# Kernel tuning notes

Measured on AMD Instinct MI355X. Metric: run time of the kernel, lower is better.

The kernel has to match this reference:

```python
import jax, jax.numpy as jnp
import numpy as np

B, S, D, K, F = 4, 2048, 1024, 4, 4096
C_COEF = 8.0  # RG-LRU gating exponent from Griffin paper
EPS = 1e-6


def setup_inputs() -> dict:
    key = jax.random.key(0)
    ks = jax.random.split(key, 12)
    def n(k, shape, scale=1.0):
        return jax.random.normal(k, shape, dtype=jnp.float32) * scale
    sd = 1.0 / np.sqrt(D)
    return {
        "x": n(ks[0], (B, S, D)),
        "velocity": n(ks[1], (B, S, D), 0.1),
        "pre_norm_w": jnp.ones((D,), jnp.float32),
        "conv_kernel": n(ks[2], (D, K), 0.3),   # depthwise causal conv weights
        "conv_bias": jnp.zeros((D,), jnp.float32),
        "W_gate": n(ks[3], (D, D), sd),
        "W_a": n(ks[4], (D, D), sd),
        "lam": n(ks[5], (D,)),
        "W_out": n(ks[6], (2 * D, D), 1.0 / np.sqrt(2 * D)),
        "b_out": jnp.zeros((D,), jnp.float32),
        "log_beta": n(ks[7], (D,), 0.5),
        "ffn_norm_w": jnp.ones((D,), jnp.float32),
        "W_ff1": n(ks[8], (D, F), sd),
        "b_ff1": jnp.zeros((F,), jnp.float32),
        "W_ff2": n(ks[9], (F, D), 1.0 / np.sqrt(F)),
        "b_ff2": jnp.zeros((D,), jnp.float32),
    }


def _rmsnorm(x, w):
    # matches: rsqrt(x.float().pow(2).mean(-1, keepdim=True) + 1e-6); cast back; * weight
    xf = x.astype(jnp.float32)
    rms = jax.lax.rsqrt(jnp.mean(xf * xf, axis=-1, keepdims=True) + EPS)
    return (xf * rms).astype(x.dtype) * w


def _causal_dwconv(x, kernel, bias):
    # y[b,t,d] = bias[d] + sum_k kernel[d,k] * x[b,t-k,d]  (causal depthwise)
    k_taps = kernel.shape[1]
    s = x.shape[1]
    pad = jnp.pad(x, ((0, 0), (k_taps - 1, 0), (0, 0)))
    out = bias
    for k in range(k_taps):  # tiny fixed loop over kernel taps
        out = out + pad[:, k_taps - 1 - k : k_taps - 1 - k + s, :] * kernel[:, k]
    return out


def _griffin_scan(x, W_gate, W_a, lam):
    # RG-LRU: h_t = a_t * h_{t-1} + sqrt(1 - a_t^2) * (i_t * x_t)
    gate = jax.nn.sigmoid(jnp.einsum("bsd,de->bse", x, W_gate))
    log_a = -C_COEF * jax.nn.softplus(lam) * jax.nn.sigmoid(
        jnp.einsum("bsd,de->bse", x, W_a)
    )  # [B,S,D], log_a <= 0
    a = jnp.exp(log_a)
    u = jnp.sqrt(jnp.maximum(1.0 - a * a, 0.0)) * (gate * x)

    def step(h, au):
        a_t, u_t = au
        h = a_t * h + u_t
        return h, h

    a_t = jnp.moveaxis(a, 1, 0)  # [S,B,D]
    u_t = jnp.moveaxis(u, 1, 0)
    h0 = jnp.zeros_like(a_t[0])
    _, hs = jax.lax.scan(step, h0, (a_t, u_t))
    return jnp.moveaxis(hs, 0, 1)  # [B,S,D]


def reference(x, velocity, pre_norm_w, conv_kernel, conv_bias, W_gate, W_a, lam,
              W_out, b_out, log_beta, ffn_norm_w, W_ff1, b_ff1, W_ff2, b_ff2):
    x_norm = _rmsnorm(x, pre_norm_w)
    conv_out = _causal_dwconv(x_norm, conv_kernel, conv_bias)
    griffin_out = _griffin_scan(x_norm, W_gate, W_a, lam)
    mixer_out = jnp.concatenate([conv_out, griffin_out], axis=-1) @ W_out + b_out
    beta = jax.nn.sigmoid(log_beta)
    velocity = beta * velocity + mixer_out
    x = x + velocity
    normed = _rmsnorm(x, ffn_norm_w)
    ffn = jax.nn.gelu(normed @ W_ff1 + b_ff1) @ W_ff2 + b_ff2
    return (x + ffn, velocity)
```

## Files before the change

kernel.cpp:

```cpp
#include <hip/hip_runtime.h>

static constexpr int Bb = 4;
static constexpr int Ss = 2048;
static constexpr int Dd = 1024;
static constexpr int Ff = 4096;
static constexpr int Mm = Bb * Ss;
static constexpr size_t ND = (size_t)Mm * Dd;
static constexpr int CH = 32;
static constexpr int CL = Ss / CH;

typedef __attribute__((ext_vector_type(8))) short short8;
typedef __attribute__((ext_vector_type(4))) float floatx4;

__device__ __forceinline__ unsigned f2bf(float f) {
  unsigned u = __builtin_bit_cast(unsigned, f);
  return (u + 0x7FFFu + ((u >> 16) & 1u)) >> 16;
}
__device__ __forceinline__ float bf2f(unsigned bits) {
  return __builtin_bit_cast(float, bits << 16);
}
__device__ __forceinline__ void gload_lds16(const void* g, void* lds) {
  __builtin_amdgcn_global_load_lds((const __attribute__((address_space(1))) void*)g,
                                   (__attribute__((address_space(3))) void*)lds,
                                   16, 0, 0);
}
__device__ __forceinline__ float fsig(float x) {
  return __builtin_amdgcn_rcpf(1.0f + __expf(-x));
}
__device__ __forceinline__ float fgelu(float v) {
  float z = 1.5957691216057308f * fmaf(0.044715f * v, v * v, v);
  return v * __builtin_amdgcn_rcpf(1.0f + __expf(-z));
}

__global__ __launch_bounds__(256) void wconv_k(const float* __restrict__ W,
                                               unsigned short* __restrict__ WT,
                                               int K, int N) {
  __shared__ float tile[32][33];
  int tx = threadIdx.x & 31, ty = threadIdx.x >> 5;
  int bx = blockIdx.x * 32, by = blockIdx.y * 32;
#pragma unroll
  for (int i = 0; i < 32; i += 8)
    tile[ty + i][tx] = W[(size_t)(by + ty + i) * N + bx + tx];
  __syncthreads();
#pragma unroll
  for (int i = 0; i < 32; i += 8)
    WT[(size_t)(bx + ty + i) * K + by + tx] = (unsigned short)f2bf(tile[tx][ty + i]);
}

__global__ __launch_bounds__(256) void rmsnorm_bf_k(const float* __restrict__ x,
                                                    const float* __restrict__ w,
                                                    unsigned short* __restrict__ out) {
  int row = blockIdx.x;
  const float4* xr = (const float4*)(x + (size_t)row * Dd);
  int t = threadIdx.x;
  float4 v = xr[t];
  float ss = v.x * v.x + v.y * v.y + v.z * v.z + v.w * v.w;
#pragma unroll
  for (int off = 32; off > 0; off >>= 1) ss += __shfl_down(ss, off, 64);
  __shared__ float sb[4];
  if ((t & 63) == 0) sb[t >> 6] = ss;
  __syncthreads();
  float tot = sb[0] + sb[1] + sb[2] + sb[3];
  float sc = rsqrtf(tot * (1.0f / (float)Dd) + 1e-6f);
  float4 wv = ((const float4*)w)[t];
  unsigned lo = f2bf(v.x * sc * wv.x) | (f2bf(v.y * sc * wv.y) << 16);
  unsigned hi = f2bf(v.z * sc * wv.z) | (f2bf(v.w * sc * wv.w) << 16);
  *(uint2*)(out + (size_t)row * Dd + t * 4) = make_uint2(lo, hi);
}

__global__ __launch_bounds__(256) void conv_k(const unsigned short* __restrict__ xn,
                                              const float* __restrict__ kern,
                                              const float* __restrict__ bias,
                                              unsigned short* __restrict__ outC) {
  size_t q = (size_t)blockIdx.x * 256 + threadIdx.x;
  size_t i = q * 4;
  int d = (int)(i & (Dd - 1));
  int m = (int)(i >> 10);
  int t = m & (Ss - 1);
  float acc[4];
#pragma unroll
  for (int j = 0; j < 4; j++) acc[j] = bias[d + j];
#pragma unroll
  for (int k = 0; k < 4; k++) {
    if (t >= k) {
      uint2 xv = *(const uint2*)(xn + i - (size_t)k * Dd);
      float x0 = bf2f(xv.x & 0xFFFF), x1 = bf2f(xv.x >> 16);
      float x2 = bf2f(xv.y & 0xFFFF), x3 = bf2f(xv.y >> 16);
      acc[0] = fmaf(kern[(d + 0) * 4 + k], x0, acc[0]);
      acc[1] = fmaf(kern[(d + 1) * 4 + k], x1, acc[1]);
      acc[2] = fmaf(kern[(d + 2) * 4 + k], x2, acc[2]);
      acc[3] = fmaf(kern[(d + 3) * 4 + k], x3, acc[3]);
    }
  }
  unsigned lo = f2bf(acc[0]) | (f2bf(acc[1]) << 16);
  unsigned hi = f2bf(acc[2]) | (f2bf(acc[3]) << 16);
  *(uint2*)(outC + (size_t)m * (2 * Dd) + d) = make_uint2(lo, hi);
}

template <int MODE>
__global__ __launch_bounds__(512, 2) void bgemm3_k(const unsigned short* __restrict__ A,
                                                   const unsigned short* __restrict__ BT,
                                                   void* __restrict__ Cout,
                                                   int M, int N, int K,
                                                   const float* __restrict__ bias,
                                                   const float* __restrict__ extra,
                                                   const float* __restrict__ vel_in,
                                                   const float* __restrict__ x_in,
                                                   const float* __restrict__ log_beta,
                                                   float* __restrict__ vel_out) {
  __shared__ unsigned short LA[2][256 * 64];
  __shared__ unsigned short LB[2][256 * 64];
  const int tid = threadIdx.x;
  const int wid = tid >> 6, lane = tid & 63;
  const int wm = wid >> 2, wn = wid & 3;
  const int r = lane & 15, quad = lane >> 4, r7 = lane & 7;

  const int gx = gridDim.x;
  int id = blockIdx.y * gx + blockIdx.x;
  const int nwg = gx * gridDim.y;
  id = (id & 7) * (nwg >> 3) + (id >> 3);
  const int bm = (id / gx) * 256, bn = (id % gx) * 256;
  const int NIT = K >> 7;

  const int lrow = lane >> 3;
  const int sblk = (lane & 7) ^ lrow;
  const unsigned short* AsrcB = A  + (size_t)(bm + lrow) * K + sblk * 8;
  const unsigned short* BsrcB = BT + (size_t)(bn + lrow) * K + sblk * 8;

  const int aB = wm * 8192 + r * 64;
  const int bB = wn * 4096 + r * 64;
  const int kq0 = (quad ^ r7) * 8;
  const int kq1 = ((4 + quad) ^ r7) * 8;

  floatx4 acc[8][4];
#pragma unroll
  for (int i = 0; i < 8; i++)
#pragma unroll
    for (int j = 0; j < 4; j++) acc[i][j] = (floatx4){0.f, 0.f, 0.f, 0.f};

#define STG_A(bq, k0, h, s)                                                           \
  gload_lds16(AsrcB + (size_t)((h) * 128 + (s) * 64 + wid * 8) * K + (k0),            \
              (void*)&LA[bq][((h) * 128 + (s) * 64 + wid * 8) * 64])
#define STG_B(bq, k0, h, s)                                                           \
  gload_lds16(BsrcB + (size_t)((h) * 128 + (s) * 64 + wid * 8) * K + (k0),            \
              (void*)&LB[bq][((h) * 128 + (s) * 64 + wid * 8) * 64])
#define RDA(il, IH, buf)                                                              \
  aF[il][0] = *(const short8*)&LA[buf][aB + (IH) * 4096 + (il) * 1024 + kq0];         \
  aF[il][1] = *(const short8*)&LA[buf][aB + (IH) * 4096 + (il) * 1024 + kq1]
#define RDB(BF, jl, jg, buf)                                                          \
  BF[jl][0] = *(const short8*)&LB[buf][bB + (jg) * 1024 + kq0];                       \
  BF[jl][1] = *(const short8*)&LB[buf][bB + (jg) * 1024 + kq1]
#define MM2(il, jl, BF, IH, JH)                                                       \
  acc[(IH) * 4 + (il)][(JH) * 2 + (jl)] = __builtin_amdgcn_mfma_f32_16x16x32_bf16(    \
      BF[jl][0], aF[il][0], acc[(IH) * 4 + (il)][(JH) * 2 + (jl)], 0, 0, 0);          \
  acc[(IH) * 4 + (il)][(JH) * 2 + (jl)] = __builtin_amdgcn_mfma_f32_16x16x32_bf16(    \
      BF[jl][1], aF[il][1], acc[(IH) * 4 + (il)][(JH) * 2 + (jl)], 0, 0, 0)
#define MQUAD(BF, IH, JH)                                                             \
  MM2(0, 0, BF, IH, JH); MM2(0, 1, BF, IH, JH); MM2(1, 0, BF, IH, JH);                \
  MM2(1, 1, BF, IH, JH); MM2(2, 0, BF, IH, JH); MM2(2, 1, BF, IH, JH);                \
  MM2(3, 0, BF, IH, JH); MM2(3, 1, BF, IH, JH)
#define BAR() __builtin_amdgcn_s_barrier()
#define LGK0()                                                                        \
  asm volatile("s_waitcnt lgkmcnt(0)" ::: "memory");                                  \
  __builtin_amdgcn_sched_barrier(0)
#define PRIO(x) __builtin_amdgcn_s_setprio(x)

  STG_A(0, 0, 0, 0); STG_A(0, 0, 0, 1); STG_A(0, 0, 1, 0); STG_A(0, 0, 1, 1);
  STG_B(0, 0, 0, 0); STG_B(0, 0, 0, 1); STG_B(0, 0, 1, 0); STG_B(0, 0, 1, 1);
  STG_B(1, 64, 0, 0); STG_B(1, 64, 0, 1); STG_B(1, 64, 1, 0); STG_B(1, 64, 1, 1);
  asm volatile("s_waitcnt vmcnt(4)" ::: "memory");
  BAR();
  __builtin_amdgcn_sched_barrier(0);

  for (int it = 0; it < NIT; ++it) {
    const int T = 2 * it;
    const int pf = (it + 1 < NIT);
    const int kA1 = (T + 1) << 6;
    const int k2 = (T + 2) << 6, k3 = (T + 3) << 6;
    short8 aF[4][2], b0[2][2], b1[2][2];

    STG_A(1, kA1, 0, 0); STG_A(1, kA1, 0, 1);
    RDA(0, 0, 0); RDA(1, 0, 0); RDA(2, 0, 0); RDA(3, 0, 0);
    RDB(b0, 0, 0, 0); RDB(b0, 1, 1, 0);
    BAR(); LGK0();
    PRIO(1); MQUAD(b0, 0, 0); PRIO(0);
    BAR();

    STG_A(1, kA1, 1, 0); STG_A(1, kA1, 1, 1);
    RDB(b1, 0, 2, 0); RDB(b1, 1, 3, 0);
    BAR(); LGK0();
    PRIO(1); MQUAD(b1, 0, 1); PRIO(0);
    BAR();

    if (pf) { STG_B(0, k2, 0, 0); STG_B(0, k2, 0, 1); }
    RDA(0, 1, 0); RDA(1, 1, 0); RDA(2, 1, 0); RDA(3, 1, 0);
    BAR(); LGK0();
    PRIO(1); MQUAD(b0, 1, 0); PRIO(0);
    BAR();

    if (pf) { STG_B(0, k2, 1, 0); STG_B(0, k2, 1, 1); }
    BAR();
    PRIO(1); MQUAD(b1, 1, 1); PRIO(0);
    if (pf) asm volatile("s_waitcnt vmcnt(4)" ::: "memory");
    else    asm volatile("s_waitcnt vmcnt(0)" ::: "memory");
    BAR();
    __builtin_amdgcn_sched_barrier(0);

    if (pf) { STG_A(0, k2, 0, 0); STG_A(0, k2, 0, 1); }
    RDA(0, 0, 1); RDA(1, 0, 1); RDA(2, 0, 1); RDA(3, 0, 1);
    RDB(b0, 0, 0, 1); RDB(b0, 1, 1, 1);
    BAR(); LGK0();
    PRIO(1); MQUAD(b0, 0, 0); PRIO(0);
    BAR();

    if (pf) { STG_A(0, k2, 1, 0); STG_A(0, k2, 1, 1); }
    RDB(b1, 0, 2, 1); RDB(b1, 1, 3, 1);
    BAR(); LGK0();
    PRIO(1); MQUAD(b1, 0, 1); PRIO(0);
    BAR();

    if (pf) { STG_B(1, k3, 0, 0); STG_B(1, k3, 0, 1); }
    RDA(0, 1, 1); RDA(1, 1, 1); RDA(2, 1, 1); RDA(3, 1, 1);
    BAR(); LGK0();
    PRIO(1); MQUAD(b0, 1, 0); PRIO(0);
    BAR();

    if (pf) { STG_B(1, k3, 1, 0); STG_B(1, k3, 1, 1); }
    BAR();
    PRIO(1); MQUAD(b1, 1, 1); PRIO(0);
    if (pf) {
      asm volatile("s_waitcnt vmcnt(4)" ::: "memory");
      BAR();
      __builtin_amdgcn_sched_barrier(0);
    }
  }
#undef STG_A
#undef STG_B
#undef RDA
#undef RDB
#undef MM2
#undef MQUAD
#undef BAR
#undef LGK0
#undef PRIO

#pragma unroll
  for (int i = 0; i < 8; i++) {
    int rowg = bm + wm * 128 + i * 16 + r;
#pragma unroll
    for (int j = 0; j < 4; j++) {
      int colg = bn + wn * 64 + j * 16 + quad * 4;
      size_t idx = (size_t)rowg * N + colg;
      float v0 = acc[i][j][0], v1 = acc[i][j][1], v2 = acc[i][j][2], v3 = acc[i][j][3];
      if (MODE & 1) {
        float4 bv = *(const float4*)(bias + colg);
        v0 += bv.x; v1 += bv.y; v2 += bv.z; v3 += bv.w;
      }
      if (MODE & 2) {
        v0 = fgelu(v0); v1 = fgelu(v1); v2 = fgelu(v2); v3 = fgelu(v3);
      }
      if (MODE & 4) {
        float4 ev = *(const float4*)(extra + idx);
        v0 += ev.x; v1 += ev.y; v2 += ev.z; v3 += ev.w;
      }
      if (MODE & 16) {
        float4 lb = *(const float4*)(log_beta + colg);
        float4 vi = *(const float4*)(vel_in + idx);
        float4 xi = *(const float4*)(x_in + idx);
        float4 vn;
        vn.x = fmaf(fsig(lb.x), vi.x, v0);
        vn.y = fmaf(fsig(lb.y), vi.y, v1);
        vn.z = fmaf(fsig(lb.z), vi.z, v2);
        vn.w = fmaf(fsig(lb.w), vi.w, v3);
        *(float4*)(vel_out + idx) = vn;
        v0 = xi.x + vn.x; v1 = xi.y + vn.y; v2 = xi.z + vn.z; v3 = xi.w + vn.w;
      }
      if (MODE & 8) {
        uint2 pk;
        pk.x = f2bf(v0) | (f2bf(v1) << 16);
        pk.y = f2bf(v2) | (f2bf(v3) << 16);
        *(uint2*)((unsigned short*)Cout + idx) = pk;
      } else {
        float4 o; o.x = v0; o.y = v1; o.z = v2; o.w = v3;
        *(float4*)((float*)Cout + idx) = o;
      }
    }
  }
}

__global__ __launch_bounds__(256) void scan_p1(const unsigned short* __restrict__ gapre,
                                               const unsigned short* __restrict__ xn,
                                               const float* __restrict__ lam,
                                               unsigned short* __restrict__ ub,
                                               float* __restrict__ carryA,
                                               float* __restrict__ carryH) {
  int g = blockIdx.x * 256 + threadIdx.x;
  int e = g & (Dd - 1);
  int bc = g >> 10;
  int b = bc & 3;
  int c = bc >> 2;
  float l = lam[e];
  float sp = fmaxf(l, 0.0f) + log1pf(__expf(-fabsf(l)));
  float m8sp = -8.0f * sp;
  size_t m0 = (size_t)b * Ss + (size_t)c * CL;
  float A = 1.0f, h = 0.0f;
#pragma unroll 4
  for (int t = 0; t < CL; t++) {
    size_t m = m0 + t;
    float gp = bf2f(gapre[m * 2048 + e]);
    float ap = bf2f(gapre[m * 2048 + 1024 + e]);
    float xv = bf2f(xn[m * Dd + e]);
    float a = __expf(m8sp * fsig(ap));
    float u = sqrtf(fmaxf(1.0f - a * a, 0.0f)) * fsig(gp) * xv;
    ub[m * Dd + e] = (unsigned short)f2bf(u);
    A *= a;
    h = fmaf(a, h, u);
  }
  carryA[c * 4096 + b * 1024 + e] = A;
  carryH[c * 4096 + b * 1024 + e] = h;
}

__global__ __launch_bounds__(256) void scan_p2(const float* __restrict__ carryA,
                                               const float* __restrict__ carryH,
                                               float* __restrict__ init) {
  int ch = blockIdx.x * 256 + threadIdx.x;
  float H = 0.0f;
#pragma unroll
  for (int c = 0; c < CH; c++) {
    init[c * 4096 + ch] = H;
    H = fmaf(carryA[c * 4096 + ch], H, carryH[c * 4096 + ch]);
  }
}

__global__ __launch_bounds__(256) void scan_p3(const unsigned short* __restrict__ gapre,
                                               const unsigned short* __restrict__ ub,
                                               const float* __restrict__ lam,
                                               const float* __restrict__ init,
                                               unsigned short* __restrict__ outC) {
  int g = blockIdx.x * 256 + threadIdx.x;
  int e = g & (Dd - 1);
  int bc = g >> 10;
  int b = bc & 3;
  int c = bc >> 2;
  float l = lam[e];
  float sp = fmaxf(l, 0.0f) + log1pf(__expf(-fabsf(l)));
  float m8sp = -8.0f * sp;
  size_t m0 = (size_t)b * Ss + (size_t)c * CL;
  float h = init[c * 4096 + b * 1024 + e];
#pragma unroll 4
  for (int t = 0; t < CL; t++) {
    size_t m = m0 + t;
    float ap = bf2f(gapre[m * 2048 + 1024 + e]);
    float a = __expf(m8sp * fsig(ap));
    float u = bf2f(ub[m * Dd + e]);
    h = fmaf(a, h, u);
    outC[m * (2 * Dd) + Dd + e] = (unsigned short)f2bf(h);
  }
}

extern "C" void kernel_launch(void* const* d_in, const int* in_sizes, int n_in,
                              void* d_out, int out_size, void* d_ws, size_t ws_size,
                              hipStream_t stream) {
  const float* x        = (const float*)d_in[0];
  const float* velocity = (const float*)d_in[1];
  const float* pre_w    = (const float*)d_in[2];
  const float* conv_w   = (const float*)d_in[3];
  const float* conv_b   = (const float*)d_in[4];
  const float* W_gate   = (const float*)d_in[5];
  const float* W_a      = (const float*)d_in[6];
  const float* lam      = (const float*)d_in[7];
  const float* W_out    = (const float*)d_in[8];
  const float* b_out    = (const float*)d_in[9];
  const float* log_beta = (const float*)d_in[10];
  const float* ffn_w    = (const float*)d_in[11];
  const float* W_ff1    = (const float*)d_in[12];
  const float* b_ff1    = (const float*)d_in[13];
  const float* W_ff2    = (const float*)d_in[14];
  const float* b_ff2    = (const float*)d_in[15];

  float* out0 = (float*)d_out;
  float* out1 = out0 + ND;

  const size_t MB = 1024 * 1024;
  char* ws = (char*)d_ws;
  unsigned short* WgaT  = (unsigned short*)ws;
  unsigned short* WoT   = WgaT + (size_t)2 * 1024 * 1024;
  unsigned short* Wf1T  = WoT + (size_t)2 * 1024 * 1024;
  unsigned short* Wf2T  = Wf1T + (size_t)4 * 1024 * 1024;
  float*          mixer = (float*)(ws + 24 * MB);
  float*          carA  = (float*)(ws + 24 * MB);
  float*          carH  = (float*)(ws + 24 * MB + 512 * 1024);
  float*          initb = (float*)(ws + 25 * MB);
  unsigned short* conc  = (unsigned short*)(ws + 56 * MB);
  unsigned short* gapre = (unsigned short*)(ws + 88 * MB);
  unsigned short* xnbf  = (unsigned short*)(ws + 120 * MB);
  unsigned short* ubf   = (unsigned short*)(ws + 136 * MB);
  unsigned short* midbf = (unsigned short*)(ws + 88 * MB);
  unsigned short* nrmbf = (unsigned short*)(ws + 56 * MB);

  const int EB = 256;
  const int egrid4 = (int)(ND / 4 / EB);

  wconv_k<<<dim3(32, 32),  256, 0, stream>>>(W_gate, WgaT, 1024, 1024);
  wconv_k<<<dim3(32, 32),  256, 0, stream>>>(W_a,    WgaT + (size_t)1024 * 1024, 1024, 1024);
  wconv_k<<<dim3(32, 64),  256, 0, stream>>>(W_out,  WoT, 2048, 1024);
  wconv_k<<<dim3(128, 32), 256, 0, stream>>>(W_ff1,  Wf1T, 1024, 4096);
  wconv_k<<<dim3(32, 128), 256, 0, stream>>>(W_ff2,  Wf2T, 4096, 1024);
  rmsnorm_bf_k<<<Mm, 256, 0, stream>>>(x, pre_w, xnbf);
  conv_k<<<egrid4, EB, 0, stream>>>(xnbf, conv_w, conv_b, conc);
  bgemm3_k<8><<<dim3(8, 32), 512, 0, stream>>>(xnbf, WgaT, gapre, Mm, 2048, 1024,
      nullptr, nullptr, nullptr, nullptr, nullptr, nullptr);
  scan_p1<<<512, 256, 0, stream>>>(gapre, xnbf, lam, ubf, carA, carH);
  scan_p2<<<16, 256, 0, stream>>>(carA, carH, initb);
  scan_p3<<<512, 256, 0, stream>>>(gapre, ubf, lam, initb, conc);
  bgemm3_k<1 | 16><<<dim3(4, 32), 512, 0, stream>>>(conc, WoT, mixer, Mm, 1024, 2048,
      b_out, nullptr, velocity, x, log_beta, out1);
  rmsnorm_bf_k<<<Mm, 256, 0, stream>>>(mixer, ffn_w, nrmbf);
  bgemm3_k<1 | 2 | 8><<<dim3(16, 32), 512, 0, stream>>>(nrmbf, Wf1T, midbf, Mm, 4096, 1024,
      b_ff1, nullptr, nullptr, nullptr, nullptr, nullptr);
  bgemm3_k<1 | 4><<<dim3(4, 32), 512, 0, stream>>>(midbf, Wf2T, out0, Mm, 1024, 4096,
      b_ff2, mixer, nullptr, nullptr, nullptr, nullptr);
}
```

Measured before the change: 653.3 us.

## Add 256x128-tile GEMM kernel for N=1024 projections to double workgroup count

Adds a new bgemm4_k variant that uses 256x128 output tiles with 4x4 accumulators per wave instead of the larger tiles of bgemm3_k. It is used for the W_out and W_ff2 GEMMs, whose N=1024 output previously gave only 128 workgroups. The goal is better occupancy and CU coverage on the many-CU GPU, since that grid underfilled the device. In exchange, each block gets less operand reuse per loaded tile and issues more global-to-LDS traffic per FLOP. The pipeline is restructured around smaller B tiles with different waitcnt accounting.

Result: faster. 587.3 us (-10.1%).

```diff
diff --git a/kernel.cpp b/kernel.cpp
--- a/kernel.cpp
+++ b/kernel.cpp
@@ -240,13 +240,197 @@
 #undef RDB
 #undef MM2
 #undef MQUAD
+
+#pragma unroll
+  for (int i = 0; i < 8; i++) {
+    int rowg = bm + wm * 128 + i * 16 + r;
+#pragma unroll
+    for (int j = 0; j < 4; j++) {
+      int colg = bn + wn * 64 + j * 16 + quad * 4;
+      size_t idx = (size_t)rowg * N + colg;
+      float v0 = acc[i][j][0], v1 = acc[i][j][1], v2 = acc[i][j][2], v3 = acc[i][j][3];
+      if (MODE & 1) {
+        float4 bv = *(const float4*)(bias + colg);
+        v0 += bv.x; v1 += bv.y; v2 += bv.z; v3 += bv.w;
+      }
+      if (MODE & 2) {
+        v0 = fgelu(v0); v1 = fgelu(v1); v2 = fgelu(v2); v3 = fgelu(v3);
+      }
+      if (MODE & 4) {
+        float4 ev = *(const float4*)(extra + idx);
+        v0 += ev.x; v1 += ev.y; v2 += ev.z; v3 += ev.w;
+      }
+      if (MODE & 16) {
+        float4 lb = *(const float4*)(log_beta + colg);
+        float4 vi = *(const float4*)(vel_in + idx);
+        float4 xi = *(const float4*)(x_in + idx);
+        float4 vn;
+        vn.x = fmaf(fsig(lb.x), vi.x, v0);
+        vn.y = fmaf(fsig(lb.y), vi.y, v1);
+        vn.z = fmaf(fsig(lb.z), vi.z, v2);
+        vn.w = fmaf(fsig(lb.w), vi.w, v3);
+        *(float4*)(vel_out + idx) = vn;
+        v0 = xi.x + vn.x; v1 = xi.y + vn.y; v2 = xi.z + vn.z; v3 = xi.w + vn.w;
+      }
+      if (MODE & 8) {
+        uint2 pk;
+        pk.x = f2bf(v0) | (f2bf(v1) << 16);
+        pk.y = f2bf(v2) | (f2bf(v3) << 16);
+        *(uint2*)((unsigned short*)Cout + idx) = pk;
+      } else {
+        float4 o; o.x = v0; o.y = v1; o.z = v2; o.w = v3;
+        *(float4*)((float*)Cout + idx) = o;
+      }
+    }
+  }
+}
+
+template <int MODE>
+__global__ __launch_bounds__(512, 2) void bgemm4_k(const unsigned short* __restrict__ A,
+                                                   const unsigned short* __restrict__ BT,
+                                                   void* __restrict__ Cout,
+                                                   int M, int N, int K,
+                                                   const float* __restrict__ bias,
+                                                   const float* __restrict__ extra,
+                                                   const float* __restrict__ vel_in,
+                                                   const float* __restrict__ x_in,
+                                                   const float* __restrict__ log_beta,
+                                                   float* __restrict__ vel_out) {
+  __shared__ unsigned short LA[2][256 * 64];
+  __shared__ unsigned short LB[2][128 * 64];
+  const int tid = threadIdx.x;
+  const int wid = tid >> 6, lane = tid & 63;
+  const int wm = wid >> 1, wn = wid & 1;
+  const int r = lane & 15, quad = lane >> 4, r7 = lane & 7;
+
+  const int gx = gridDim.x;
+  int id = blockIdx.y * gx + blockIdx.x;
+  const int nwg = gx * gridDim.y;
+  id = (id & 7) * (nwg >> 3) + (id >> 3);
+  const int bm = (id / gx) * 256, bn = (id % gx) * 128;
+  const int NIT = K >> 7;
+
+  const int lrow = lane >> 3;
+  const int sblk = (lane & 7) ^ lrow;
+  const unsigned short* AsrcB = A  + (size_t)(bm + lrow) * K + sblk * 8;
+  const unsigned short* BsrcB = BT + (size_t)(bn + lrow) * K + sblk * 8;
+
+  const int aB = wm * 4096 + r * 64;
+  const int bB = wn * 4096 + r * 64;
+  const int kq0 = (quad ^ r7) * 8;
+  const int kq1 = ((4 + quad) ^ r7) * 8;
+
+  floatx4 acc[4][4];
+#pragma unroll
+  for (int i = 0; i < 4; i++)
+#pragma unroll
+    for (int j = 0; j < 4; j++) acc[i][j] = (floatx4){0.f, 0.f, 0.f, 0.f};
+
+#define STG_A4(bq, k0, h, s)                                                          \
+  gload_lds16(AsrcB + (size_t)((h) * 128 + (s) * 64 + wid * 8) * K + (k0),            \
+              (void*)&LA[bq][((h) * 128 + (s) * 64 + wid * 8) * 64])
+#define STG_B4(bq, k0, s)                                                             \
+  gload_lds16(BsrcB + (size_t)((s) * 64 + wid * 8) * K + (k0),                        \
+              (void*)&LB[bq][((s) * 64 + wid * 8) * 64])
+#define RDA4(IH, buf)                                                                 \
+  aF[0][0] = *(const short8*)&LA[buf][aB + (IH) * 2048 + kq0];                        \
+  aF[0][1] = *(const short8*)&LA[buf][aB + (IH) * 2048 + kq1];                        \
+  aF[1][0] = *(const short8*)&LA[buf][aB + (IH) * 2048 + 1024 + kq0];                 \
+  aF[1][1] = *(const short8*)&LA[buf][aB + (IH) * 2048 + 1024 + kq1]
+#define RDB4(BF, JH, buf)                                                             \
+  BF[0][0] = *(const short8*)&LB[buf][bB + (JH) * 2048 + kq0];                        \
+  BF[0][1] = *(const short8*)&LB[buf][bB + (JH) * 2048 + kq1];                        \
+  BF[1][0] = *(const short8*)&LB[buf][bB + (JH) * 2048 + 1024 + kq0];                 \
+  BF[1][1] = *(const short8*)&LB[buf][bB + (JH) * 2048 + 1024 + kq1]
+#define MM24(il, jl, BF, IH, JH)                                                      \
+  acc[(IH) * 2 + (il)][(JH) * 2 + (jl)] = __builtin_amdgcn_mfma_f32_16x16x32_bf16(    \
+      BF[jl][0], aF[il][0], acc[(IH) * 2 + (il)][(JH) * 2 + (jl)], 0, 0, 0);          \
+  acc[(IH) * 2 + (il)][(JH) * 2 + (jl)] = __builtin_amdgcn_mfma_f32_16x16x32_bf16(    \
+      BF[jl][1], aF[il][1], acc[(IH) * 2 + (il)][(JH) * 2 + (jl)], 0, 0, 0)
+#define MQ4(BF, IH, JH)                                                               \
+  MM24(0, 0, BF, IH, JH); MM24(0, 1, BF, IH, JH);                                     \
+  MM24(1, 0, BF, IH, JH); MM24(1, 1, BF, IH, JH)
+
+  STG_A4(0, 0, 0, 0); STG_A4(0, 0, 0, 1); STG_A4(0, 0, 1, 0); STG_A4(0, 0, 1, 1);
+  STG_B4(0, 0, 0); STG_B4(0, 0, 1);
+  STG_B4(1, 64, 0); STG_B4(1, 64, 1);
+  asm volatile("s_waitcnt vmcnt(2)" ::: "memory");
+  BAR();
+  __builtin_amdgcn_sched_barrier(0);
+
+  for (int it = 0; it < NIT; ++it) {
+    const int T = 2 * it;
+    const int pf = (it + 1 < NIT);
+    const int kA1 = (T + 1) << 6;
+    const int k2 = (T + 2) << 6, k3 = (T + 3) << 6;
+    short8 aF[2][2], b0[2][2], b1[2][2];
+
+    STG_A4(1, kA1, 0, 0); STG_A4(1, kA1, 0, 1);
+    RDA4(0, 0); RDB4(b0, 0, 0);
+    BAR(); LGK0();
+    PRIO(1); MQ4(b0, 0, 0); PRIO(0);
+    BAR();
+
+    STG_A4(1, kA1, 1, 0); STG_A4(1, kA1, 1, 1);
+    RDB4(b1, 1, 0);
+    BAR(); LGK0();
+    PRIO(1); MQ4(b1, 0, 1); PRIO(0);
+    BAR();
+
+    if (pf) STG_B4(0, k2, 0);
+    RDA4(1, 0);
+    BAR(); LGK0();
+    PRIO(1); MQ4(b0, 1, 0); PRIO(0);
+    BAR();
+
+    if (pf) STG_B4(0, k2, 1);
+    BAR();
+    PRIO(1); MQ4(b1, 1, 1); PRIO(0);
+    if (pf) asm volatile("s_waitcnt vmcnt(2)" ::: "memory");
+    else    asm volatile("s_waitcnt vmcnt(0)" ::: "memory");
+    BAR();
+    __builtin_amdgcn_sched_barrier(0);
+
+    if (pf) { STG_A4(0, k2, 0, 0); STG_A4(0, k2, 0, 1); }
+    RDA4(0, 1); RDB4(b0, 0, 1);
+    BAR(); LGK0();
+    PRIO(1); MQ4(b0, 0, 0); PRIO(0);
+    BAR();
+
+    if (pf) { STG_A4(0, k2, 1, 0); STG_A4(0, k2, 1, 1); }
+    RDB4(b1, 1, 1);
+    BAR(); LGK0();
+    PRIO(1); MQ4(b1, 0, 1); PRIO(0);
+    BAR();
+
+    if (pf) STG_B4(1, k3, 0);
+    RDA4(1, 1);
+    BAR(); LGK0();
+    PRIO(1); MQ4(b0, 1, 0); PRIO(0);
+    BAR();
+
+    if (pf) STG_B4(1, k3, 1);
+    BAR();
+    PRIO(1); MQ4(b1, 1, 1); PRIO(0);
+    if (pf) {
+      asm volatile("s_waitcnt vmcnt(2)" ::: "memory");
+      BAR();
+      __builtin_amdgcn_sched_barrier(0);
+    }
+  }
+#undef STG_A4
+#undef STG_B4
+#undef RDA4
+#undef RDB4
+#undef MM24
+#undef MQ4
 #undef BAR
 #undef LGK0
 #undef PRIO
 
 #pragma unroll
-  for (int i = 0; i < 8; i++) {
-    int rowg = bm + wm * 128 + i * 16 + r;
+  for (int i = 0; i < 4; i++) {
+    int rowg = bm + wm * 64 + i * 16 + r;
 #pragma unroll
     for (int j = 0; j < 4; j++) {
       int colg = bn + wn * 64 + j * 16 + quad * 4;
@@ -413,11 +597,11 @@
   scan_p1<<<512, 256, 0, stream>>>(gapre, xnbf, lam, ubf, carA, carH);
   scan_p2<<<16, 256, 0, stream>>>(carA, carH, initb);
   scan_p3<<<512, 256, 0, stream>>>(gapre, ubf, lam, initb, conc);
-  bgemm3_k<1 | 16><<<dim3(4, 32), 512, 0, stream>>>(conc, WoT, mixer, Mm, 1024, 2048,
+  bgemm4_k<1 | 16><<<dim3(8, 32), 512, 0, stream>>>(conc, WoT, mixer, Mm, 1024, 2048,
       b_out, nullptr, velocity, x, log_beta, out1);
   rmsnorm_bf_k<<<Mm, 256, 0, stream>>>(mixer, ffn_w, nrmbf);
   bgemm3_k<1 | 2 | 8><<<dim3(16, 32), 512, 0, stream>>>(nrmbf, Wf1T, midbf, Mm, 4096, 1024,
       b_ff1, nullptr, nullptr, nullptr, nullptr, nullptr);
-  bgemm3_k<1 | 4><<<dim3(4, 32), 512, 0, stream>>>(midbf, Wf2T, out0, Mm, 1024, 4096,
+  bgemm4_k<1 | 4><<<dim3(8, 32), 512, 0, stream>>>(midbf, Wf2T, out0, Mm, 1024, 4096,
       b_ff2, mixer, nullptr, nullptr, nullptr, nullptr);
 }
```
